# Performance work log

Measured on AMD Instinct MI355X. Metric: run time of the kernel, lower is better.

## Reference

```python
import jax, jax.numpy as jnp
import numpy as np
import math

SHIFTS = (1, 2, 4, 8)
EPS_IN = 1e-5  # InstanceNorm2d eps
EPS_BN = 1e-5  # BatchNorm2d eps

def _eight_shifts(x, d):
    # Reproduces DATrans.feature_padding: 8 reflection-padded shifted views.
    H, W = x.shape[-2], x.shape[-1]
    def p(rt, rb, cl, cr):
        return jnp.pad(x, ((0, 0), (0, 0), (rt, rb), (cl, cr)), mode='reflect')
    return [
        p(d, 0, d, 0)[..., :H, :W],   # left-top
        p(d, 0, 0, 0)[..., :H, :],    # center-top
        p(d, 0, 0, d)[..., :H, d:],   # right-top
        p(0, 0, d, 0)[..., :, :W],    # left-center
        p(0, 0, 0, d)[..., :, d:],    # right-center
        p(0, d, d, 0)[..., d:, :W],   # left-bottom
        p(0, d, 0, 0)[..., d:, :],    # center-bottom
        p(0, d, 0, d)[..., d:, d:],   # right-bottom
    ]

def _l2n(x):
    # torch F.normalize(dim=-1, eps=1e-12)
    return x / jnp.maximum(jnp.linalg.norm(x, axis=-1, keepdims=True), 1e-12)

def setup_inputs() -> dict:
    key = jax.random.key(0)
    ks = jax.random.split(key, 9)
    B, Cin, H, W = 4, 16, 256, 256
    heads, hidden, NL, Cout = 4, 16, 8, 16
    tra = heads * hidden
    cen = jax.random.normal(ks[0], (B, Cin, H, W), jnp.float32)
    q_w = jax.random.normal(ks[1], (heads, hidden, Cin), jnp.float32) / np.sqrt(Cin).astype(np.float32)
    k_w = jax.random.normal(ks[2], (heads, hidden * NL, Cin * NL), jnp.float32) / np.sqrt(Cin * NL).astype(np.float32)
    v_w = jax.random.normal(ks[3], (heads, hidden * NL, Cin * NL), jnp.float32) / np.sqrt(Cin * NL).astype(np.float32)
    out_w = jax.random.normal(ks[4], (Cout, tra), jnp.float32) / np.sqrt(tra).astype(np.float32)
    bn_gamma = jax.random.uniform(ks[5], (Cout,), jnp.float32) + 0.5
    bn_beta = jax.random.normal(ks[6], (Cout,), jnp.float32) * 0.1
    bn_mean = jax.random.normal(ks[7], (Cout,), jnp.float32) * 0.1
    bn_var = jax.random.uniform(ks[8], (Cout,), jnp.float32) + 0.5
    return dict(cen=cen, q_w=q_w, k_w=k_w, v_w=v_w, out_w=out_w,
                bn_gamma=bn_gamma, bn_beta=bn_beta, bn_mean=bn_mean, bn_var=bn_var)

def reference(cen, q_w, k_w, v_w, out_w, bn_gamma, bn_beta, bn_mean, bn_var):
    b, Cin, H, W = cen.shape
    area = H * W
    heads = len(SHIFTS)
    qs, ksl, vsl = [], [], []
    for i, d in enumerate(SHIFTS):  # small fixed loop over heads
        sur = jnp.concatenate([s - cen for s in _eight_shifts(cen, d)], axis=1)  # [b, 8*Cin, H, W]
        ksl.append(jnp.einsum('oc,bchw->bohw', k_w[i], sur))  # 1x1 conv, no bias
        vsl.append(jnp.einsum('oc,bchw->bohw', v_w[i], sur))
        qs.append(jnp.einsum('oc,bchw->bohw', q_w[i], cen))
    # torch stack(dim=2).view(b, heads, -1, area) on contiguous tensor == stack+reshape
    K = jnp.stack(ksl, axis=2).reshape(b, heads, -1, area)  # [b, heads, 8*hid, area]
    Q = jnp.stack(qs, axis=2).reshape(b, heads, -1, area)   # [b, heads, hid, area]
    V = jnp.stack(vsl, axis=2).reshape(b, heads, -1, area)
    scores = jnp.einsum('bhca,bhda->bhcd', _l2n(Q), _l2n(K)) / math.sqrt(area)  # [b,h,hid,8*hid]
    # InstanceNorm2d(heads): per (b, head) over last two dims, no affine
    mu = scores.mean(axis=(-2, -1), keepdims=True)
    var = scores.var(axis=(-2, -1), keepdims=True)
    attn = jax.nn.softmax((scores - mu) * jax.lax.rsqrt(var + EPS_IN), axis=-1)
    out = jnp.einsum('bhcd,bhda->bhca', attn, V)  # [b, heads, hid, area]
    tra = out.shape[1] * out.shape[2]
    out = out.reshape(b, tra, H, W)
    out = jnp.einsum('oc,bchw->bohw', out_w, out)  # out_conv 1x1, no bias
    g = bn_gamma[None, :, None, None]
    bta = bn_beta[None, :, None, None]
    m = bn_mean[None, :, None, None]
    v = bn_var[None, :, None, None]
    out = (out - m) * jax.lax.rsqrt(v + EPS_BN) * g + bta  # eval-mode BatchNorm2d
    return jax.nn.relu(out)
```

## Files before the change

kernel.cpp:

```cpp
#include <hip/hip_runtime.h>
#include <hip/hip_bf16.h>
#include <math.h>

#define HH 256
#define WW 256
#define AREA 65536
#define CIN 16
#define NS 4
#define CSUR 128
#define NEXT 144
#define NPAIR 45

typedef __attribute__((ext_vector_type(8))) short bf16x8;
typedef __attribute__((ext_vector_type(4))) float f32x4;

__constant__ int c_dy[8] = {-1,-1,-1, 0, 0, 1, 1, 1};
__constant__ int c_dx[8] = {-1, 0, 1,-1, 1,-1, 0, 1};

__device__ constexpr int CTI[NPAIR] = {
    0, 1,1, 2,2,2, 3,3,3,3, 4,4,4,4,4,
    5,5,5,5,5,5, 6,6,6,6,6,6,6, 7,7,7,7,7,7,7,7,
    8,8,8,8,8,8,8,8,8};
__device__ constexpr int CTJ[NPAIR] = {
    0, 0,1, 0,1,2, 0,1,2,3, 0,1,2,3,4,
    0,1,2,3,4,5, 0,1,2,3,4,5,6, 0,1,2,3,4,5,6,7,
    0,1,2,3,4,5,6,7,8};

__device__ __forceinline__ int refl(int v) {
    return v < 0 ? -v : (v > 255 ? 510 - v : v);
}

__device__ __forceinline__ unsigned pkbf(float a, float b) {
    __hip_bfloat162 h = __float22bfloat162_rn(make_float2(a, b));
    unsigned r;
    __builtin_memcpy(&r, &h, 4);
    return r;
}

__device__ __forceinline__ void wp(unsigned* __restrict__ m,
                                   int c, int pxp, float a, float b) {
    const int base = c * 32, sw = c & 7, gi = pxp >> 2, e = pxp & 3;
    const unsigned h = pkbf(a, b);
    m[base + ((gi ^ sw) << 2) + e] = h;
    const float fa = __builtin_bit_cast(float, h << 16);
    const float fb = __builtin_bit_cast(float, h & 0xFFFF0000u);
    m[base + (((4 + gi) ^ sw) << 2) + e] = pkbf(a - fa, b - fb);
}

template <bool FAST>
__device__ __forceinline__ void stage_tile(unsigned* __restrict__ m,
                                           const float* __restrict__ base,
                                           int y, int x0, int cin, int pxp, int d) {
    constexpr int DY[8] = {-1,-1,-1, 0, 0, 1, 1, 1};
    constexpr int DX[8] = {-1, 0, 1,-1, 1,-1, 0, 1};
    const int x = x0 + 2 * pxp;
    const float2 cv = *(const float2*)(base + y * WW + x);
    wp(m, cin, pxp, cv.x, cv.y);
#pragma unroll
    for (int kk = 0; kk < 8; ++kk) {
        float2 sv;
        if (FAST) {
            const float* row = base + (y + DY[kk] * d) * WW;
            sv = *(const float2*)(row + x + DX[kk] * d);
        } else {
            const int ys  = refl(y + DY[kk] * d);
            const int xs0 = refl(x + DX[kk] * d);
            const int xs1 = refl(x + 1 + DX[kk] * d);
            const float* row = base + ys * WW;
            sv.x = row[xs0];
            sv.y = row[xs1];
        }
        wp(m, 16 + kk * 16 + cin, pxp, sv.x - cv.x, sv.y - cv.y);
    }
}

__global__ __launch_bounds__(256) void k1_gram(const float* __restrict__ cen,
                                               float* __restrict__ part) {
    const int chunk = blockIdx.x;
    const int s = blockIdx.y;
    const int b = blockIdx.z;
    const int d = 1 << s;
    const int t = threadIdx.x;
    const int lane = t & 63, wid = t >> 6;
    const int lr = lane & 15, lg = lane >> 4;
    const int cin = t >> 4, pxp = t & 15;
    const int y0 = chunk * 4;
    const float* base = cen + ((size_t)b * CIN + cin) * AREA;

    __shared__ unsigned lds[NEXT * 32];

    const int ghi = ((lg ^ (lr & 7)) << 2);
    const int glo = (((4 + lg) ^ (lr & 7)) << 2);

    f32x4 acc[12];
#pragma unroll
    for (int i = 0; i < 12; ++i) acc[i] = (f32x4){0.f, 0.f, 0.f, 0.f};

    for (int st = 0; st < 32; ++st) {
        const int y  = y0 + (st >> 3);
        const int x0 = (st & 7) * 32;
        if (y >= 8 && y <= 247 && x0 >= 32 && x0 <= 192)
            stage_tile<true>(lds, base, y, x0, cin, pxp, d);
        else
            stage_tile<false>(lds, base, y, x0, cin, pxp, d);
        __syncthreads();
        bf16x8 fh[9], fl[9];
#pragma unroll
        for (int tt = 0; tt < 9; ++tt) {
            const int rb = (tt * 16 + lr) * 32;
            fh[tt] = *(const bf16x8*)(lds + rb + ghi);
            fl[tt] = *(const bf16x8*)(lds + rb + glo);
        }
        __syncthreads();
#pragma unroll
        for (int p = 0; p < NPAIR; ++p) {
            if ((p & 3) == wid) {
                const int i = CTI[p], j = CTJ[p], a = p >> 2;
                acc[a] = __builtin_amdgcn_mfma_f32_16x16x32_bf16(fh[i], fh[j], acc[a], 0, 0, 0);
                acc[a] = __builtin_amdgcn_mfma_f32_16x16x32_bf16(fh[i], fl[j], acc[a], 0, 0, 0);
                acc[a] = __builtin_amdgcn_mfma_f32_16x16x32_bf16(fl[i], fh[j], acc[a], 0, 0, 0);
            }
        }
    }

    float* tb = part + (size_t)((chunk & 3) * 16 + b * 4 + s) * 20736;
#pragma unroll
    for (int p = 0; p < NPAIR; ++p) {
        if ((p & 3) == wid) {
            const int gi0 = CTI[p] * 16 + lg * 4;
            const int gj  = CTJ[p] * 16 + lr;
            const f32x4 a = acc[p >> 2];
#pragma unroll
            for (int r = 0; r < 4; ++r)
                atomicAdd(&tb[(gi0 + r) * 144 + gj], a[r]);
        }
    }
}

__global__ __launch_bounds__(256) void kA(const float* __restrict__ part,
                                          const float* __restrict__ q_w,
                                          const float* __restrict__ k_w,
                                          float* __restrict__ A,
                                          float* __restrict__ normK,
                                          float* __restrict__ normQ) {
    const int s = blockIdx.x, b = blockIdx.y, z = blockIdx.z, bs = b * 4 + s;
    const int t = threadIdx.x;
    const int i0 = z * 16;
    __shared__ float Ts[16][148];
    __shared__ float kwS[128][129];
    __shared__ float red[2][128];

    const float* p0 = part + (size_t)(0 * 16 + bs) * 20736;
    const float* p1 = part + (size_t)(1 * 16 + bs) * 20736;
    const float* p2 = part + (size_t)(2 * 16 + bs) * 20736;
    const float* p3 = part + (size_t)(3 * 16 + bs) * 20736;
    for (int e = t; e < 16 * 144; e += 256) {
        const int il = e / 144, j = e - il * 144;
        const int i = i0 + il;
        const int src = (i >= j) ? (i * 144 + j) : (j * 144 + i);
        Ts[il][j] = p0[src] + p1[src] + p2[src] + p3[src];
    }
    if (z >= 1) {
        const float* kws = k_w + (size_t)s * 16384;
        for (int e = t; e < 16384; e += 256)
            kwS[e >> 7][e & 127] = kws[e];
    }
    __syncthreads();

    if (z >= 1) {
        for (int e = t; e < 1024; e += 256) {
            const int il = e >> 6, jq = e & 63;
            const float* qr = q_w + jq * 16;
            float aa = 0.f;
#pragma unroll
            for (int c = 0; c < 16; ++c) aa = fmaf(qr[c], Ts[il][c], aa);
            A[((size_t)bs * 64 + jq) * 128 + (i0 - 16 + il)] = aa;
        }
        const int ck = t & 127, half = t >> 7;
        float accil[16];
#pragma unroll
        for (int il = 0; il < 16; ++il) accil[il] = 0.f;
        for (int j = half * 64; j < half * 64 + 64; ++j) {
            const float kj = kwS[ck][j];
#pragma unroll
            for (int il = 0; il < 16; ++il)
                accil[il] = fmaf(kj, Ts[il][16 + j], accil[il]);
        }
        float prt = 0.f;
#pragma unroll
        for (int il = 0; il < 16; ++il)
            prt = fmaf(kwS[ck][i0 - 16 + il], accil[il], prt);
        red[half][ck] = prt;
        __syncthreads();
        if (t < 128)
            atomicAdd(&normK[(size_t)bs * 128 + t], red[0][t] + red[1][t]);
    } else if (s == 0 && t < 64) {
        float nq = 0.f;
#pragma unroll
        for (int c1 = 0; c1 < 16; ++c1) {
            float ra = 0.f;
#pragma unroll
            for (int c2 = 0; c2 < 16; ++c2)
                ra = fmaf(q_w[t * 16 + c2], Ts[c1][c2], ra);
            nq = fmaf(q_w[t * 16 + c1], ra, nq);
        }
        normQ[b * 64 + t] = nq;
    }
}

__global__ __launch_bounds__(256) void kB(const float* __restrict__ k_w,
                                          const float* __restrict__ v_w,
                                          const float* __restrict__ A,
                                          const float* __restrict__ normK,
                                          const float* __restrict__ normQ,
                                          float* __restrict__ wEff) {
    const int a = blockIdx.x, b = blockIdx.y;
    const int t = threadIdx.x;
    __shared__ float AS[4][16][128];
    __shared__ float kv[4][32][132];
    __shared__ float sc[2048];
    __shared__ float red[256];
    __shared__ float rowred[256];
    __shared__ float rowmax[16], rowsum[16];
    __shared__ float s_mu, s_rs;

    for (int idx = t; idx < 8192; idx += 256) {
        const int sk = idx >> 11, rr = (idx >> 7) & 15, cp = idx & 127;
        const int jq = (rr & 3) * 16 + 4 * a + (rr >> 2);
        AS[sk][rr][cp] = A[((size_t)(b * 4 + sk) * 64 + jq) * 128 + cp];
    }
    for (int idx = t; idx < 16384; idx += 256) {
        const int sk = idx >> 12, ckl = (idx >> 7) & 31, cp = idx & 127;
        kv[sk][ckl][cp] = k_w[((size_t)sk * 128 + 32 * a + ckl) * 128 + cp];
    }
    __syncthreads();
    for (int e = t; e < 2048; e += 256) {
        const int r = e >> 7, dd = e & 127;
        const int sk = dd & 3, ckl = dd >> 2;
        const float4* Ar = (const float4*)(&AS[sk][r][0]);
        const float4* kr = (const float4*)(&kv[sk][ckl][0]);
        float4 pv = {0.f, 0.f, 0.f, 0.f};
#pragma unroll 8
        for (int jj = 0; jj < 32; ++jj) {
            const float4 h = Ar[jj], k4 = kr[jj];
            pv.x = fmaf(h.x, k4.x, pv.x);
            pv.y = fmaf(h.y, k4.y, pv.y);
            pv.z = fmaf(h.z, k4.z, pv.z);
            pv.w = fmaf(h.w, k4.w, pv.w);
        }
        const float dot = pv.x + pv.y + pv.z + pv.w;
        const int jq = (r & 3) * 16 + 4 * a + (r >> 2);
        const float qn = fmaxf(sqrtf(fmaxf(normQ[b * 64 + jq], 0.f)), 1e-12f);
        const float kn = fmaxf(sqrtf(fmaxf(normK[(size_t)(b * 4 + sk) * 128 + 32 * a + ckl], 0.f)), 1e-12f);
        sc[e] = dot / (qn * kn * 256.0f);
    }
    __syncthreads();
    for (int idx = t; idx < 16384; idx += 256) {
        const int sk = idx >> 12, m = (idx >> 7) & 31, cp = idx & 127;
        kv[sk][m][cp] = v_w[((size_t)sk * 128 + 32 * a + m) * 128 + cp];
    }
    {
        float p = 0.f;
        for (int e = t; e < 2048; e += 256) p += sc[e];
        red[t] = p; __syncthreads();
        for (int off = 128; off > 0; off >>= 1) {
            if (t < off) red[t] += red[t + off];
            __syncthreads();
        }
        if (t == 0) s_mu = red[0] * (1.f / 2048.f);
        __syncthreads();
    }
    {
        const float mu = s_mu;
        float p = 0.f;
        for (int e = t; e < 2048; e += 256) { const float z = sc[e] - mu; p += z * z; }
        red[t] = p; __syncthreads();
        for (int off = 128; off > 0; off >>= 1) {
            if (t < off) red[t] += red[t + off];
            __syncthreads();
        }
        if (t == 0) s_rs = rsqrtf(red[0] * (1.f / 2048.f) + 1e-5f);
        __syncthreads();
    }
    const float mu = s_mu, rs = s_rs;
    const int r = t >> 4, l = t & 15;
    {
        float m = -1e30f;
#pragma unroll
        for (int j = 0; j < 8; ++j) {
            const float z = (sc[r * 128 + l + j * 16] - mu) * rs;
            m = fmaxf(m, z);
        }
        rowred[t] = m; __syncthreads();
        if (l == 0) {
            float m2 = rowred[r * 16];
            for (int j = 1; j < 16; ++j) m2 = fmaxf(m2, rowred[r * 16 + j]);
            rowmax[r] = m2;
        }
        __syncthreads();
    }
    {
        float p = 0.f;
#pragma unroll
        for (int j = 0; j < 8; ++j) {
            const float z = (sc[r * 128 + l + j * 16] - mu) * rs;
            p += expf(z - rowmax[r]);
        }
        rowred[t] = p; __syncthreads();
        if (l == 0) {
            float p2 = 0.f;
            for (int j = 0; j < 16; ++j) p2 += rowred[r * 16 + j];
            rowsum[r] = p2;
        }
        __syncthreads();
    }
    {
        float vals[8];
#pragma unroll
        for (int j = 0; j < 8; ++j) {
            const float z = (sc[r * 128 + l + j * 16] - mu) * rs;
            vals[j] = expf(z - rowmax[r]) / rowsum[r];
        }
        __syncthreads();
#pragma unroll
        for (int j = 0; j < 8; ++j) sc[r * 128 + l + j * 16] = vals[j];
        __syncthreads();
    }
    for (int e = t; e < 8192; e += 256) {
        const int sk = e >> 11, r2 = (e >> 7) & 15, cp = e & 127;
        float w = 0.f;
#pragma unroll
        for (int m = 0; m < 32; ++m)
            w = fmaf(sc[r2 * 128 + 4 * m + sk], kv[sk][m][cp], w);
        wEff[((size_t)(b * 4 + sk) * 64 + (a * 16 + r2)) * 128 + cp] = w;
    }
}

__global__ __launch_bounds__(256) void k2c(const float* __restrict__ out_w,
                                           const float* __restrict__ bn_gamma,
                                           const float* __restrict__ bn_var,
                                           const float* __restrict__ wEff,
                                           float* __restrict__ wFinal) {
    const int s = blockIdx.x, b = blockIdx.y;
    const int t = threadIdx.x;
    __shared__ float we[64][128];
    for (int idx = t; idx < 8192; idx += 256) {
        const int j = idx >> 7, cp = idx & 127;
        we[j][cp] = wEff[((size_t)(b * 4 + s) * 64 + j) * 128 + cp];
    }
    __syncthreads();
    for (int e = t; e < 2048; e += 256) {
        const int o = e >> 7, cp = e & 127;
        float w = 0.f;
#pragma unroll 16
        for (int j = 0; j < 64; ++j)
            w = fmaf(out_w[o * 64 + j], we[j][cp], w);
        const float scale = bn_gamma[o] * rsqrtf(bn_var[o] + 1e-5f);
        wFinal[((size_t)(b * 4 + s) * 16 + o) * 128 + cp] = w * scale;
    }
}

__global__ __launch_bounds__(256) void k3_out(const float* __restrict__ cen,
                                              const float* __restrict__ wFinal,
                                              const float* __restrict__ bn_gamma,
                                              const float* __restrict__ bn_beta,
                                              const float* __restrict__ bn_mean,
                                              const float* __restrict__ bn_var,
                                              float* __restrict__ out) {
    const int by = blockIdx.x;
    const int b  = blockIdx.y;
    const int t  = threadIdx.x;
    __shared__ __align__(16) float wf[NS * CSUR * 16];
    __shared__ __align__(16) float wc[16 * 16];

    for (int e = t; e < NS * CSUR * 16; e += 256) {
        const int s = e >> 11, cp = (e >> 4) & 127, o = e & 15;
        wf[e] = wFinal[((size_t)(b * NS + s) * 16 + o) * CSUR + cp];
    }
    __syncthreads();
    {
        const int cin = t >> 4, o = t & 15;
        float sum = 0.f;
#pragma unroll
        for (int s = 0; s < NS; ++s)
#pragma unroll
            for (int k = 0; k < 8; ++k)
                sum += wf[(s * CSUR + k * 16 + cin) * 16 + o];
        wc[cin * 16 + o] = sum;
    }
    __syncthreads();

    const int x0 = t & 127;
    const int x1 = x0 + 128;
    const int y  = by * 2 + (t >> 7);
    const float* cb = cen + (size_t)b * CIN * AREA;

    float acc0[16], acc1[16];
#pragma unroll
    for (int o = 0; o < 16; ++o) { acc0[o] = 0.f; acc1[o] = 0.f; }

    for (int s = 0; s < NS; ++s) {
        const int d = 1 << s;
        for (int k = 0; k < 8; ++k) {
            const int ry  = refl(y + c_dy[k] * d);
            const int rx0 = refl(x0 + c_dx[k] * d);
            const int rx1 = refl(x1 + c_dx[k] * d);
            const float* crow = cb + ry * WW;
#pragma unroll
            for (int cin = 0; cin < 16; ++cin) {
                const float v0 = crow[cin * AREA + rx0];
                const float v1 = crow[cin * AREA + rx1];
                const float4* w4 = reinterpret_cast<const float4*>(&wf[(s * CSUR + k * 16 + cin) * 16]);
#pragma unroll
                for (int oq = 0; oq < 4; ++oq) {
                    const float4 w = w4[oq];
                    acc0[oq*4+0] = fmaf(w.x, v0, acc0[oq*4+0]); acc1[oq*4+0] = fmaf(w.x, v1, acc1[oq*4+0]);
                    acc0[oq*4+1] = fmaf(w.y, v0, acc0[oq*4+1]); acc1[oq*4+1] = fmaf(w.y, v1, acc1[oq*4+1]);
                    acc0[oq*4+2] = fmaf(w.z, v0, acc0[oq*4+2]); acc1[oq*4+2] = fmaf(w.z, v1, acc1[oq*4+2]);
                    acc0[oq*4+3] = fmaf(w.w, v0, acc0[oq*4+3]); acc1[oq*4+3] = fmaf(w.w, v1, acc1[oq*4+3]);
                }
            }
        }
    }
    {
        const float* crow = cb + y * WW;
#pragma unroll
        for (int cin = 0; cin < 16; ++cin) {
            const float v0 = crow[cin * AREA + x0];
            const float v1 = crow[cin * AREA + x1];
            const float4* w4 = reinterpret_cast<const float4*>(&wc[cin * 16]);
#pragma unroll
            for (int oq = 0; oq < 4; ++oq) {
                const float4 w = w4[oq];
                acc0[oq*4+0] = fmaf(-w.x, v0, acc0[oq*4+0]); acc1[oq*4+0] = fmaf(-w.x, v1, acc1[oq*4+0]);
                acc0[oq*4+1] = fmaf(-w.y, v0, acc0[oq*4+1]); acc1[oq*4+1] = fmaf(-w.y, v1, acc1[oq*4+1]);
                acc0[oq*4+2] = fmaf(-w.z, v0, acc0[oq*4+2]); acc1[oq*4+2] = fmaf(-w.z, v1, acc1[oq*4+2]);
                acc0[oq*4+3] = fmaf(-w.w, v0, acc0[oq*4+3]); acc1[oq*4+3] = fmaf(-w.w, v1, acc1[oq*4+3]);
            }
        }
    }
#pragma unroll
    for (int o = 0; o < 16; ++o) {
        const float scale = bn_gamma[o] * rsqrtf(bn_var[o] + 1e-5f);
        const float bias  = bn_beta[o] - bn_mean[o] * scale;
        const float r0 = fmaxf(acc0[o] + bias, 0.f);
        const float r1 = fmaxf(acc1[o] + bias, 0.f);
        out[((size_t)(b * 16 + o) * HH + y) * WW + x0] = r0;
        out[((size_t)(b * 16 + o) * HH + y) * WW + x1] = r1;
    }
}

extern "C" void kernel_launch(void* const* d_in, const int* in_sizes, int n_in,
                              void* d_out, int out_size, void* d_ws, size_t ws_size,
                              hipStream_t stream) {
    const float* cen      = (const float*)d_in[0];
    const float* q_w      = (const float*)d_in[1];
    const float* k_w      = (const float*)d_in[2];
    const float* v_w      = (const float*)d_in[3];
    const float* out_w    = (const float*)d_in[4];
    const float* bn_gamma = (const float*)d_in[5];
    const float* bn_beta  = (const float*)d_in[6];
    const float* bn_mean  = (const float*)d_in[7];
    const float* bn_var   = (const float*)d_in[8];
    float* out = (float*)d_out;

    char* ws = (char*)d_ws;
    const size_t PART_BYTES  = (size_t)4 * 16 * 20736 * 4;
    const size_t NK_BYTES    = (size_t)16 * 128 * 4;
    const size_t A_BYTES     = (size_t)16 * 64 * 128 * 4;
    const size_t NQ_BYTES    = (size_t)4 * 64 * 4;
    const size_t WEFF_BYTES  = (size_t)16 * 64 * 128 * 4;

    float* part  = (float*)(ws);
    float* normK = (float*)(ws + PART_BYTES);
    float* A     = (float*)(ws + PART_BYTES + NK_BYTES);
    float* normQ = (float*)(ws + PART_BYTES + NK_BYTES + A_BYTES);
    float* wEff  = (float*)(ws + PART_BYTES + NK_BYTES + A_BYTES + NQ_BYTES);
    float* wFin  = (float*)(ws + PART_BYTES + NK_BYTES + A_BYTES + NQ_BYTES + WEFF_BYTES);

    (void)hipMemsetAsync(part, 0, PART_BYTES + NK_BYTES, stream);
    k1_gram<<<dim3(64, 4, 4), 256, 0, stream>>>(cen, part);
    kA<<<dim3(4, 4, 9), 256, 0, stream>>>(part, q_w, k_w, A, normK, normQ);
    kB<<<dim3(4, 4), 256, 0, stream>>>(k_w, v_w, A, normK, normQ, wEff);
    k2c<<<dim3(4, 4), 256, 0, stream>>>(out_w, bn_gamma, bn_var, wEff, wFin);
    k3_out<<<dim3(128, 4), 256, 0, stream>>>(cen, wFin, bn_gamma, bn_beta,
                                             bn_mean, bn_var, out);
}
```

Baseline: 295.9 us.

## Replace split-bf16 Gram MFMAs with single fp16 MFMAs over wider tiles

The Gram-matrix kernel now converts inputs to fp16 with a single packed round-toward-zero conversion, replacing the bf16 hi/lo split that needed three MFMAs per tile pair. The freed LDS half is used to stage 64 pixels per round instead of 32, so the loop runs 16 rounds with two MFMAs each instead of 32 rounds with three. This halves barriers and cuts MFMA count by a third. In exchange it gives up precision: fp16 has fewer mantissa bits than the split-bf16 scheme, uses RTZ rounding, and can overflow on large differences.

```diff
diff --git a/kernel.cpp b/kernel.cpp
--- a/kernel.cpp
+++ b/kernel.cpp
@@ -1,5 +1,4 @@
 #include <hip/hip_runtime.h>
-#include <hip/hip_bf16.h>
 #include <math.h>
 
 #define HH 256
@@ -11,7 +10,7 @@
 #define NEXT 144
 #define NPAIR 45
 
-typedef __attribute__((ext_vector_type(8))) short bf16x8;
+typedef __attribute__((ext_vector_type(8))) _Float16 f16x8;
 typedef __attribute__((ext_vector_type(4))) float f32x4;
 
 __constant__ int c_dy[8] = {-1,-1,-1, 0, 0, 1, 1, 1};
@@ -30,47 +29,49 @@
     return v < 0 ? -v : (v > 255 ? 510 - v : v);
 }
 
-__device__ __forceinline__ unsigned pkbf(float a, float b) {
-    __hip_bfloat162 h = __float22bfloat162_rn(make_float2(a, b));
-    unsigned r;
-    __builtin_memcpy(&r, &h, 4);
-    return r;
-}
-
-__device__ __forceinline__ void wp(unsigned* __restrict__ m,
-                                   int c, int pxp, float a, float b) {
-    const int base = c * 32, sw = c & 7, gi = pxp >> 2, e = pxp & 3;
-    const unsigned h = pkbf(a, b);
-    m[base + ((gi ^ sw) << 2) + e] = h;
-    const float fa = __builtin_bit_cast(float, h << 16);
-    const float fb = __builtin_bit_cast(float, h & 0xFFFF0000u);
-    m[base + (((4 + gi) ^ sw) << 2) + e] = pkbf(a - fa, b - fb);
+__device__ __forceinline__ unsigned pkh(float a, float b) {
+    auto h2 = __builtin_amdgcn_cvt_pkrtz(a, b);
+    return __builtin_bit_cast(unsigned, h2);
+}
+
+__device__ __forceinline__ void wph(unsigned* __restrict__ m,
+                                    int c, int pxp, int halfk, float a, float b) {
+    const int sw = c & 7, gi = halfk * 4 + (pxp >> 2), e = pxp & 3;
+    m[c * 32 + ((gi ^ sw) << 2) + e] = pkh(a, b);
 }
 
 template <bool FAST>
-__device__ __forceinline__ void stage_tile(unsigned* __restrict__ m,
-                                           const float* __restrict__ base,
-                                           int y, int x0, int cin, int pxp, int d) {
+__device__ __forceinline__ void stage64(unsigned* __restrict__ m,
+                                        const float* __restrict__ base,
+                                        int y, int x0, int cin, int pxp, int d) {
     constexpr int DY[8] = {-1,-1,-1, 0, 0, 1, 1, 1};
     constexpr int DX[8] = {-1, 0, 1,-1, 1,-1, 0, 1};
-    const int x = x0 + 2 * pxp;
-    const float2 cv = *(const float2*)(base + y * WW + x);
-    wp(m, cin, pxp, cv.x, cv.y);
+    const int xA = x0 + 2 * pxp;
+    const int xB = xA + 32;
+    const float* rowy = base + y * WW;
+    const float2 cA = *(const float2*)(rowy + xA);
+    const float2 cB = *(const float2*)(rowy + xB);
+    wph(m, cin, pxp, 0, cA.x, cA.y);
+    wph(m, cin, pxp, 1, cB.x, cB.y);
 #pragma unroll
     for (int kk = 0; kk < 8; ++kk) {
-        float2 sv;
+        float2 sA, sB;
         if (FAST) {
             const float* row = base + (y + DY[kk] * d) * WW;
-            sv = *(const float2*)(row + x + DX[kk] * d);
+            sA = *(const float2*)(row + xA + DX[kk] * d);
+            sB = *(const float2*)(row + xB + DX[kk] * d);
         } else {
-            const int ys  = refl(y + DY[kk] * d);
-            const int xs0 = refl(x + DX[kk] * d);
-            const int xs1 = refl(x + 1 + DX[kk] * d);
+            const int ys = refl(y + DY[kk] * d);
             const float* row = base + ys * WW;
-            sv.x = row[xs0];
-            sv.y = row[xs1];
-        }
-        wp(m, 16 + kk * 16 + cin, pxp, sv.x - cv.x, sv.y - cv.y);
+            const int off = DX[kk] * d;
+            sA.x = row[refl(xA + off)];
+            sA.y = row[refl(xA + 1 + off)];
+            sB.x = row[refl(xB + off)];
+            sB.y = row[refl(xB + 1 + off)];
+        }
+        const int c = 16 + kk * 16 + cin;
+        wph(m, c, pxp, 0, sA.x - cA.x, sA.y - cA.y);
+        wph(m, c, pxp, 1, sB.x - cB.x, sB.y - cB.y);
     }
 }
 
@@ -89,36 +90,35 @@
 
     __shared__ unsigned lds[NEXT * 32];
 
-    const int ghi = ((lg ^ (lr & 7)) << 2);
-    const int glo = (((4 + lg) ^ (lr & 7)) << 2);
+    const int rA = ((lg ^ (lr & 7)) << 2);
+    const int rB = (((4 + lg) ^ (lr & 7)) << 2);
 
     f32x4 acc[12];
 #pragma unroll
     for (int i = 0; i < 12; ++i) acc[i] = (f32x4){0.f, 0.f, 0.f, 0.f};
 
-    for (int st = 0; st < 32; ++st) {
-        const int y  = y0 + (st >> 3);
-        const int x0 = (st & 7) * 32;
-        if (y >= 8 && y <= 247 && x0 >= 32 && x0 <= 192)
-            stage_tile<true>(lds, base, y, x0, cin, pxp, d);
+    for (int rd = 0; rd < 16; ++rd) {
+        const int y  = y0 + (rd >> 2);
+        const int x0 = (rd & 3) * 64;
+        if (y >= 8 && y <= 247 && x0 >= 64 && x0 <= 128)
+            stage64<true>(lds, base, y, x0, cin, pxp, d);
         else
-            stage_tile<false>(lds, base, y, x0, cin, pxp, d);
-        __syncthreads();
-        bf16x8 fh[9], fl[9];
+            stage64<false>(lds, base, y, x0, cin, pxp, d);
+        __syncthreads();
+        f16x8 fA[9], fB[9];
 #pragma unroll
         for (int tt = 0; tt < 9; ++tt) {
             const int rb = (tt * 16 + lr) * 32;
-            fh[tt] = *(const bf16x8*)(lds + rb + ghi);
-            fl[tt] = *(const bf16x8*)(lds + rb + glo);
+            fA[tt] = __builtin_bit_cast(f16x8, *(const uint4*)(lds + rb + rA));
+            fB[tt] = __builtin_bit_cast(f16x8, *(const uint4*)(lds + rb + rB));
         }
         __syncthreads();
 #pragma unroll
         for (int p = 0; p < NPAIR; ++p) {
             if ((p & 3) == wid) {
                 const int i = CTI[p], j = CTJ[p], a = p >> 2;
-                acc[a] = __builtin_amdgcn_mfma_f32_16x16x32_bf16(fh[i], fh[j], acc[a], 0, 0, 0);
-                acc[a] = __builtin_amdgcn_mfma_f32_16x16x32_bf16(fh[i], fl[j], acc[a], 0, 0, 0);
-                acc[a] = __builtin_amdgcn_mfma_f32_16x16x32_bf16(fl[i], fh[j], acc[a], 0, 0, 0);
+                acc[a] = __builtin_amdgcn_mfma_f32_16x16x32_f16(fA[i], fA[j], acc[a], 0, 0, 0);
+                acc[a] = __builtin_amdgcn_mfma_f32_16x16x32_f16(fB[i], fB[j], acc[a], 0, 0, 0);
             }
         }
     }
```

Result: faster. 260.1 us (-12.1%).
